# Optimization experiments

Hardware: AMD Instinct MI355X
Metric: run time of the kernel (lower is better)

The kernel has to match this reference:

```python
import jax, jax.numpy as jnp
import numpy as np

B, T, L, D, U = 2048, 500, 128, 64, 128  # batch, time steps, latent_dim, output_dim, n_units


def setup_inputs() -> dict:
    key = jax.random.key(0)
    ks = jax.random.split(key, 10)
    def init(k, shape, fan_in):
        return jax.random.uniform(k, shape, jnp.float32, -1.0, 1.0) / np.sqrt(fan_in)
    return {
        "first_point": jax.random.normal(ks[0], (1, B, L), jnp.float32),
        "time_steps_to_predict": jnp.arange(T, dtype=jnp.float32),
        # GRUCell params (torch layout: weight [3*hidden, in], gates ordered r,z,n)
        "w_ih": init(ks[1], (3 * L, D + 1), L),
        "w_hh": init(ks[2], (3 * L, L), L),
        "b_ih": init(ks[3], (3 * L,), L),
        "b_hh": init(ks[4], (3 * L,), L),
        # output_net: Linear(L,U) -> tanh -> Linear(U,D)
        "w1": init(ks[5], (U, L), L),
        "b1": jnp.zeros((U,), jnp.float32),
        "w2": init(ks[6], (D, U), U),
        "b2": jnp.zeros((D,), jnp.float32),
    }


def _gru_cell(x, h, w_ih, w_hh, b_ih, b_hh):
    gi = x @ w_ih.T + b_ih  # [B, 3L]
    gh = h @ w_hh.T + b_hh  # [B, 3L]
    i_r, i_z, i_n = jnp.split(gi, 3, axis=-1)
    h_r, h_z, h_n = jnp.split(gh, 3, axis=-1)
    r = jax.nn.sigmoid(i_r + h_r)
    z = jax.nn.sigmoid(i_z + h_z)
    n = jnp.tanh(i_n + r * h_n)
    return (1.0 - z) * n + z * h


def reference(first_point, time_steps_to_predict, w_ih, w_hh, b_ih, b_hh, w1, b1, w2, b2):
    def mlp(h):
        return jnp.tanh(h @ w1.T + b1) @ w2.T + b2  # [B, D]

    ts = time_steps_to_predict
    delta_ts = jnp.concatenate([jnp.zeros((1,), ts.dtype), ts[1:] - ts[:-1]])  # [T]

    h0 = first_point[0]          # [B, L]
    p0 = mlp(h0)                 # [B, D]
    batch = h0.shape[0]

    def step(carry, dt):
        h, p = carry
        dt_col = jnp.broadcast_to(dt.reshape(1, 1), (batch, 1))
        x = jnp.concatenate([p, dt_col], axis=-1)  # [B, D+1]
        h = _gru_cell(x, h, w_ih, w_hh, b_ih, b_hh)
        p = mlp(h)
        return (h, p), (h, p)

    _, (hs, ps) = jax.lax.scan(step, (h0, p0), delta_ts[1:])  # [T-1, B, *]
    sol_z = jnp.concatenate([h0[None], hs], axis=0)   # [T, B, L]
    pred_x = jnp.concatenate([p0[None], ps], axis=0)  # [T, B, D]
    sol_z = jnp.transpose(sol_z, (1, 0, 2))[None]     # [1, B, T, L]
    pred_x = jnp.transpose(pred_x, (1, 0, 2))[None]   # [1, B, T, D]
    return sol_z, pred_x
```

## Files before the change

kernel.cpp:

```cpp
#include <hip/hip_runtime.h>

#define BB 2048
#define TT 500
#define LL 128
#define DD 64
#define UU 128

using f16x8 = __attribute__((ext_vector_type(8))) _Float16;
using f32x4 = __attribute__((ext_vector_type(4))) float;

__device__ __forceinline__ float bf2f(unsigned short u){
  union { unsigned u; float f; } v; v.u = ((unsigned)u) << 16; return v.f;
}
__device__ __forceinline__ unsigned short f2bf(float f){
  union { float f; unsigned u; } v; v.f = f;
  unsigned r = v.u + 0x7FFFu + ((v.u >> 16) & 1u);
  return (unsigned short)(r >> 16);
}
__device__ __forceinline__ float cvt(unsigned short v){ return bf2f(v); }
__device__ __forceinline__ float cvt(float v){ return v; }

__device__ __forceinline__ float exp2_(float x){
  float r; asm("v_exp_f32 %0, %1" : "=v"(r) : "v"(x)); return r;
}

__device__ __forceinline__ void bar_lds(){
  asm volatile("s_waitcnt lgkmcnt(0)\n\ts_barrier" ::: "memory");
}

#define C1 (-1.44269504088896340736f)
#define C2 ( 2.88539008177792681472f)

#define SH 136
#define SA 136

struct Frags {
  f16x8 Wc[3][4];
  f16x8 Wh[3][4];
  f16x8 W1f[4];
  f16x8 W2f[4];
  float br, bz, bin, bhn, wdr, wdz, wdn, b1c, b2c;
};

template <typename T>
__device__ __forceinline__ void preload(
    const void* wih_, const void* whh_, const void* bih_, const void* bhh_,
    const void* w1_, const void* b1_, const void* w2_, const void* b2_,
    int c, int lq, Frags& F)
{
  const T* wih = (const T*)wih_; const T* whh = (const T*)whh_;
  const T* bih = (const T*)bih_; const T* bhh = (const T*)bhh_;
  const T* w1  = (const T*)w1_;  const T* b1  = (const T*)b1_;
  const T* w2  = (const T*)w2_;  const T* b2  = (const T*)b2_;
  const float gs[3] = {C1, C1, C2};
  #pragma unroll
  for (int g = 0; g < 3; ++g){
    const int row = g*128 + c;
    #pragma unroll
    for (int kt = 0; kt < 4; ++kt)
      #pragma unroll
      for (int j = 0; j < 8; ++j)
        F.Wh[g][kt][j] = (_Float16)(gs[g]*cvt(whh[row*128 + kt*32 + lq*8 + j]));
  }
  #pragma unroll
  for (int kt = 0; kt < 4; ++kt)
    #pragma unroll
    for (int j = 0; j < 8; ++j)
      F.W1f[kt][j] = (_Float16)(C2*cvt(w1[c*128 + kt*32 + lq*8 + j]));
  const int c2 = c & 63;
  #pragma unroll
  for (int kt = 0; kt < 4; ++kt)
    #pragma unroll
    for (int j = 0; j < 8; ++j)
      F.W2f[kt][j] = (_Float16)cvt(w2[c2*128 + kt*32 + lq*8 + j]);

  for (int kt = 0; kt < 4; ++kt){
    float acc[3][8];
    #pragma unroll
    for (int g = 0; g < 3; ++g)
      #pragma unroll
      for (int j = 0; j < 8; ++j) acc[g][j] = 0.f;
    for (int d = 0; d < 64; ++d){
      float w2r[8];
      #pragma unroll
      for (int j = 0; j < 8; ++j)
        w2r[j] = cvt(w2[d*128 + kt*32 + lq*8 + j]);
      #pragma unroll
      for (int g = 0; g < 3; ++g){
        const float wpv = cvt(wih[(g*128 + c)*65 + d]);
        #pragma unroll
        for (int j = 0; j < 8; ++j) acc[g][j] += wpv * w2r[j];
      }
    }
    #pragma unroll
    for (int g = 0; g < 3; ++g)
      #pragma unroll
      for (int j = 0; j < 8; ++j)
        F.Wc[g][kt][j] = (_Float16)(gs[g]*acc[g][j]);
  }
  float bc[3] = {0.f, 0.f, 0.f};
  for (int d = 0; d < 64; ++d){
    const float b2v = cvt(b2[d]);
    #pragma unroll
    for (int g = 0; g < 3; ++g)
      bc[g] += cvt(wih[(g*128 + c)*65 + d]) * b2v;
  }
  F.br  = C1*(cvt(bih[c])     + cvt(bhh[c])     + bc[0]);
  F.bz  = C1*(cvt(bih[128+c]) + cvt(bhh[128+c]) + bc[1]);
  F.bin = C2*(cvt(bih[256+c]) + bc[2]);
  F.bhn = C2*cvt(bhh[256+c]);
  F.wdr = C1*cvt(wih[c*65 + 64]);
  F.wdz = C1*cvt(wih[(128+c)*65 + 64]);
  F.wdn = C2*cvt(wih[(256+c)*65 + 64]);
  F.b1c = C2*cvt(b1[c]);
  F.b2c = cvt(b2[c2]);
}

__global__ __launch_bounds__(512, 2) void rnn_decoder(
    const void* __restrict__ fp0,
    const void* __restrict__ ts,
    const void* __restrict__ wih,
    const void* __restrict__ whh,
    const void* __restrict__ bih,
    const void* __restrict__ bhh,
    const void* __restrict__ w1,
    const void* __restrict__ b1,
    const void* __restrict__ w2,
    const void* __restrict__ b2,
    void* __restrict__ out)
{
  __shared__ __align__(16) _Float16 sh[16*SH];
  __shared__ __align__(16) _Float16 sa[16*SA];
  __shared__ float dts[TT];

  const int tid  = threadIdx.x;
  const int wv   = tid >> 6;
  const int lane = tid & 63;
  const int lm   = lane & 15;
  const int lq   = lane >> 4;
  const int b0   = blockIdx.x << 4;
  const int c    = (wv << 4) + lm;

  const bool isbf = (((const unsigned*)ts)[1] != 0x3F800000u);

  Frags F;
  if (isbf) preload<unsigned short>(wih, whh, bih, bhh, w1, b1, w2, b2, c, lq, F);
  else      preload<float>         (wih, whh, bih, bhh, w1, b1, w2, b2, c, lq, F);

  if (isbf){
    const unsigned short* t16 = (const unsigned short*)ts;
    for (int t = tid; t < TT; t += 512)
      dts[t] = t ? (bf2f(t16[t]) - bf2f(t16[t-1])) : 0.f;
  } else {
    const float* t32 = (const float*)ts;
    for (int t = tid; t < TT; t += 512)
      dts[t] = t ? (t32[t] - t32[t-1]) : 0.f;
  }

  unsigned short* outh16 = (unsigned short*)out;
  unsigned short* outp16 = outh16 + (size_t)BB*TT*LL;
  float* outh32 = (float*)out;
  float* outp32 = outh32 + (size_t)BB*TT*LL;

  unsigned offh[4], offp[4];
  #pragma unroll
  for (int i = 0; i < 4; ++i){
    offh[i] = (unsigned)((b0 + lq*4 + i)*TT*LL + c) + (unsigned)LL;
    offp[i] = (unsigned)((b0 + lq*4 + i)*TT*DD + (c & 63));
  }

  {
    const int row = tid >> 5;
    const int k4  = (tid & 31) << 2;
    if (isbf){
      const unsigned short* src = (const unsigned short*)fp0 + (b0 + row)*LL + k4;
      ushort4 v = *(const ushort4*)src;
      #pragma unroll
      for (int j = 0; j < 4; ++j)
        sh[row*SH + k4 + j] = (_Float16)bf2f(((const unsigned short*)&v)[j]);
      *(ushort4*)(outh16 + (size_t)(b0 + row)*TT*LL + k4) = v;
    } else {
      const float* src = (const float*)fp0 + (b0 + row)*LL + k4;
      float4 v = *(const float4*)src;
      sh[row*SH + k4 + 0] = (_Float16)v.x;
      sh[row*SH + k4 + 1] = (_Float16)v.y;
      sh[row*SH + k4 + 2] = (_Float16)v.z;
      sh[row*SH + k4 + 3] = (_Float16)v.w;
      *(float4*)(outh32 + (size_t)(b0 + row)*TT*LL + k4) = v;
    }
  }
  bar_lds();

  float hprev[4];
  #pragma unroll
  for (int i = 0; i < 4; ++i)
    hprev[i] = (float)sh[(lq*4 + i)*SH + c];

  f16x8 ahc[4], aac[4];
  #pragma unroll
  for (int kt = 0; kt < 4; ++kt)
    ahc[kt] = *(const f16x8*)&sh[lm*SH + kt*32 + lq*8];

  f32x4 aR = {0,0,0,0}, aZ = {0,0,0,0}, aH = {0,0,0,0};
  {
    f32x4 acc = {0,0,0,0};
    #pragma unroll
    for (int kt = 0; kt < 4; ++kt)
      acc = __builtin_amdgcn_mfma_f32_16x16x32_f16(ahc[kt], F.W1f[kt], acc, 0,0,0);
    #pragma unroll
    for (int kt = 0; kt < 4; ++kt){
      aR = __builtin_amdgcn_mfma_f32_16x16x32_f16(ahc[kt], F.Wh[0][kt], aR, 0,0,0);
      aZ = __builtin_amdgcn_mfma_f32_16x16x32_f16(ahc[kt], F.Wh[1][kt], aZ, 0,0,0);
      aH = __builtin_amdgcn_mfma_f32_16x16x32_f16(ahc[kt], F.Wh[2][kt], aH, 0,0,0);
    }
    #pragma unroll
    for (int i = 0; i < 4; ++i)
      sa[(lq*4 + i)*SA + c] =
        (_Float16)(1.f - 2.f*__builtin_amdgcn_rcpf(1.f + exp2_(acc[i] + F.b1c)));
  }
  bar_lds();
  #pragma unroll
  for (int kt = 0; kt < 4; ++kt)
    aac[kt] = *(const f16x8*)&sa[lm*SA + kt*32 + lq*8];

  for (int t = 1; t < TT; ++t){
    const float dt = dts[t];
    f32x4 aN = {0,0,0,0};
    #pragma unroll
    for (int kt = 0; kt < 4; ++kt){
      aR = __builtin_amdgcn_mfma_f32_16x16x32_f16(aac[kt], F.Wc[0][kt], aR, 0,0,0);
      aZ = __builtin_amdgcn_mfma_f32_16x16x32_f16(aac[kt], F.Wc[1][kt], aZ, 0,0,0);
      aN = __builtin_amdgcn_mfma_f32_16x16x32_f16(aac[kt], F.Wc[2][kt], aN, 0,0,0);
    }
    f32x4 aP = {0,0,0,0};
    if (wv < 4){
      #pragma unroll
      for (int kt = 0; kt < 4; ++kt)
        aP = __builtin_amdgcn_mfma_f32_16x16x32_f16(aac[kt], F.W2f[kt], aP, 0,0,0);
    }
    const float rb = F.br + dt*F.wdr;
    const float zb = F.bz + dt*F.wdz;
    const float nb = F.bin + dt*F.wdn;
    float hnew[4];
    #pragma unroll
    for (int i = 0; i < 4; ++i){
      const float r = __builtin_amdgcn_rcpf(1.f + exp2_(aR[i] + rb));
      const float z = __builtin_amdgcn_rcpf(1.f + exp2_(aZ[i] + zb));
      const float y = aN[i] + nb + r*(aH[i] + F.bhn);
      const float n = 1.f - 2.f*__builtin_amdgcn_rcpf(1.f + exp2_(y));
      hnew[i] = n + z*(hprev[i] - n);
      hprev[i] = hnew[i];
    }
    #pragma unroll
    for (int i = 0; i < 4; ++i)
      sh[(lq*4 + i)*SH + c] = (_Float16)hnew[i];
    bar_lds();
    #pragma unroll
    for (int kt = 0; kt < 4; ++kt)
      ahc[kt] = *(const f16x8*)&sh[lm*SH + kt*32 + lq*8];
    f32x4 acc = {0,0,0,0};
    #pragma unroll
    for (int kt = 0; kt < 4; ++kt)
      acc = __builtin_amdgcn_mfma_f32_16x16x32_f16(ahc[kt], F.W1f[kt], acc, 0,0,0);
    if (!isbf){
      #pragma unroll
      for (int i = 0; i < 4; ++i)
        outh32[offh[i]] = hnew[i];
      if (wv < 4){
        #pragma unroll
        for (int i = 0; i < 4; ++i)
          outp32[offp[i]] = aP[i] + F.b2c;
      }
    } else {
      #pragma unroll
      for (int i = 0; i < 4; ++i)
        outh16[offh[i]] = f2bf(hnew[i]);
      if (wv < 4){
        #pragma unroll
        for (int i = 0; i < 4; ++i)
          outp16[offp[i]] = f2bf(aP[i] + F.b2c);
      }
    }
    #pragma unroll
    for (int i = 0; i < 4; ++i){ offh[i] += LL; offp[i] += DD; }
    aR = (f32x4){0,0,0,0}; aZ = (f32x4){0,0,0,0}; aH = (f32x4){0,0,0,0};
    #pragma unroll
    for (int kt = 0; kt < 4; ++kt){
      aR = __builtin_amdgcn_mfma_f32_16x16x32_f16(ahc[kt], F.Wh[0][kt], aR, 0,0,0);
      aZ = __builtin_amdgcn_mfma_f32_16x16x32_f16(ahc[kt], F.Wh[1][kt], aZ, 0,0,0);
      aH = __builtin_amdgcn_mfma_f32_16x16x32_f16(ahc[kt], F.Wh[2][kt], aH, 0,0,0);
    }
    #pragma unroll
    for (int i = 0; i < 4; ++i)
      sa[(lq*4 + i)*SA + c] =
        (_Float16)(1.f - 2.f*__builtin_amdgcn_rcpf(1.f + exp2_(acc[i] + F.b1c)));
    bar_lds();
    #pragma unroll
    for (int kt = 0; kt < 4; ++kt)
      aac[kt] = *(const f16x8*)&sa[lm*SA + kt*32 + lq*8];
  }

  if (wv < 4){
    f32x4 aP = {0,0,0,0};
    #pragma unroll
    for (int kt = 0; kt < 4; ++kt)
      aP = __builtin_amdgcn_mfma_f32_16x16x32_f16(aac[kt], F.W2f[kt], aP, 0,0,0);
    if (!isbf){
      #pragma unroll
      for (int i = 0; i < 4; ++i)
        outp32[offp[i]] = aP[i] + F.b2c;
    } else {
      #pragma unroll
      for (int i = 0; i < 4; ++i)
        outp16[offp[i]] = f2bf(aP[i] + F.b2c);
    }
  }
}

extern "C" void kernel_launch(void* const* d_in, const int* in_sizes, int n_in,
                              void* d_out, int out_size, void* d_ws, size_t ws_size,
                              hipStream_t stream) {
  (void)in_sizes; (void)n_in; (void)out_size; (void)d_ws; (void)ws_size;
  rnn_decoder<<<dim3(BB/16), dim3(512), 0, stream>>>(
      d_in[0],
      d_in[1],
      d_in[2],
      d_in[3],
      d_in[4],
      d_in[5],
      d_in[6],
      d_in[7],
      d_in[8],
      d_in[9],
      d_out);
}
```

Measured before the change: 1.297 ms.

## Halve block to 4 waves, each wave computing two 16-column hidden tiles

Each block now runs 256 threads instead of 512, and each wave owns two column tiles of the hidden state (c0 and c0+64). All four waves now compute the output projection, so the wave<4 predicate is gone. The aim is to cut barrier participants and idle waves per step and to improve per-wave MFMA issue density. In exchange each wave holds twice the weight fragments in registers, which raises register pressure and allows only one block per CU via launch bounds, so there is less latency hiding.

```diff
diff --git a/kernel.cpp b/kernel.cpp
--- a/kernel.cpp
+++ b/kernel.cpp
@@ -4,7 +4,6 @@
 #define TT 500
 #define LL 128
 #define DD 64
-#define UU 128
 
 using f16x8 = __attribute__((ext_vector_type(8))) _Float16;
 using f32x4 = __attribute__((ext_vector_type(4))) float;
@@ -35,18 +34,18 @@
 #define SA 136
 
 struct Frags {
-  f16x8 Wc[3][4];
-  f16x8 Wh[3][4];
-  f16x8 W1f[4];
+  f16x8 Wc[3][2][4];
+  f16x8 Wh[3][2][4];
+  f16x8 W1f[2][4];
   f16x8 W2f[4];
-  float br, bz, bin, bhn, wdr, wdz, wdn, b1c, b2c;
+  float br[2], bz[2], bin[2], bhn[2], wdr[2], wdz[2], wdn[2], b1c[2], b2c;
 };
 
 template <typename T>
 __device__ __forceinline__ void preload(
     const void* wih_, const void* whh_, const void* bih_, const void* bhh_,
     const void* w1_, const void* b1_, const void* w2_, const void* b2_,
-    int c, int lq, Frags& F)
+    int c0, int lq, Frags& F)
 {
   const T* wih = (const T*)wih_; const T* whh = (const T*)whh_;
   const T* bih = (const T*)bih_; const T* bhh = (const T*)bhh_;
@@ -54,69 +53,72 @@
   const T* w2  = (const T*)w2_;  const T* b2  = (const T*)b2_;
   const float gs[3] = {C1, C1, C2};
   #pragma unroll
-  for (int g = 0; g < 3; ++g){
-    const int row = g*128 + c;
+  for (int ta = 0; ta < 2; ++ta){
+    const int c = c0 + 64*ta;
+    #pragma unroll
+    for (int g = 0; g < 3; ++g){
+      const int row = g*128 + c;
+      #pragma unroll
+      for (int kt = 0; kt < 4; ++kt)
+        #pragma unroll
+        for (int j = 0; j < 8; ++j)
+          F.Wh[g][ta][kt][j] = (_Float16)(gs[g]*cvt(whh[row*128 + kt*32 + lq*8 + j]));
+    }
     #pragma unroll
     for (int kt = 0; kt < 4; ++kt)
       #pragma unroll
       for (int j = 0; j < 8; ++j)
-        F.Wh[g][kt][j] = (_Float16)(gs[g]*cvt(whh[row*128 + kt*32 + lq*8 + j]));
+        F.W1f[ta][kt][j] = (_Float16)(C2*cvt(w1[c*128 + kt*32 + lq*8 + j]));
+
+    for (int kt = 0; kt < 4; ++kt){
+      float acc[3][8];
+      #pragma unroll
+      for (int g = 0; g < 3; ++g)
+        #pragma unroll
+        for (int j = 0; j < 8; ++j) acc[g][j] = 0.f;
+      for (int d = 0; d < 64; ++d){
+        float w2r[8];
+        #pragma unroll
+        for (int j = 0; j < 8; ++j)
+          w2r[j] = cvt(w2[d*128 + kt*32 + lq*8 + j]);
+        #pragma unroll
+        for (int g = 0; g < 3; ++g){
+          const float wpv = cvt(wih[(g*128 + c)*65 + d]);
+          #pragma unroll
+          for (int j = 0; j < 8; ++j) acc[g][j] += wpv * w2r[j];
+        }
+      }
+      #pragma unroll
+      for (int g = 0; g < 3; ++g)
+        #pragma unroll
+        for (int j = 0; j < 8; ++j)
+          F.Wc[g][ta][kt][j] = (_Float16)(gs[g]*acc[g][j]);
+    }
+    float bc[3] = {0.f, 0.f, 0.f};
+    for (int d = 0; d < 64; ++d){
+      const float b2v = cvt(b2[d]);
+      #pragma unroll
+      for (int g = 0; g < 3; ++g)
+        bc[g] += cvt(wih[(g*128 + c)*65 + d]) * b2v;
+    }
+    F.br[ta]  = C1*(cvt(bih[c])     + cvt(bhh[c])     + bc[0]);
+    F.bz[ta]  = C1*(cvt(bih[128+c]) + cvt(bhh[128+c]) + bc[1]);
+    F.bin[ta] = C2*(cvt(bih[256+c]) + bc[2]);
+    F.bhn[ta] = C2*cvt(bhh[256+c]);
+    F.wdr[ta] = C1*cvt(wih[c*65 + 64]);
+    F.wdz[ta] = C1*cvt(wih[(128+c)*65 + 64]);
+    F.wdn[ta] = C2*cvt(wih[(256+c)*65 + 64]);
+    F.b1c[ta] = C2*cvt(b1[c]);
   }
   #pragma unroll
   for (int kt = 0; kt < 4; ++kt)
     #pragma unroll
     for (int j = 0; j < 8; ++j)
-      F.W1f[kt][j] = (_Float16)(C2*cvt(w1[c*128 + kt*32 + lq*8 + j]));
-  const int c2 = c & 63;
-  #pragma unroll
-  for (int kt = 0; kt < 4; ++kt)
-    #pragma unroll
-    for (int j = 0; j < 8; ++j)
-      F.W2f[kt][j] = (_Float16)cvt(w2[c2*128 + kt*32 + lq*8 + j]);
-
-  for (int kt = 0; kt < 4; ++kt){
-    float acc[3][8];
-    #pragma unroll
-    for (int g = 0; g < 3; ++g)
-      #pragma unroll
-      for (int j = 0; j < 8; ++j) acc[g][j] = 0.f;
-    for (int d = 0; d < 64; ++d){
-      float w2r[8];
-      #pragma unroll
-      for (int j = 0; j < 8; ++j)
-        w2r[j] = cvt(w2[d*128 + kt*32 + lq*8 + j]);
-      #pragma unroll
-      for (int g = 0; g < 3; ++g){
-        const float wpv = cvt(wih[(g*128 + c)*65 + d]);
-        #pragma unroll
-        for (int j = 0; j < 8; ++j) acc[g][j] += wpv * w2r[j];
-      }
-    }
-    #pragma unroll
-    for (int g = 0; g < 3; ++g)
-      #pragma unroll
-      for (int j = 0; j < 8; ++j)
-        F.Wc[g][kt][j] = (_Float16)(gs[g]*acc[g][j]);
-  }
-  float bc[3] = {0.f, 0.f, 0.f};
-  for (int d = 0; d < 64; ++d){
-    const float b2v = cvt(b2[d]);
-    #pragma unroll
-    for (int g = 0; g < 3; ++g)
-      bc[g] += cvt(wih[(g*128 + c)*65 + d]) * b2v;
-  }
-  F.br  = C1*(cvt(bih[c])     + cvt(bhh[c])     + bc[0]);
-  F.bz  = C1*(cvt(bih[128+c]) + cvt(bhh[128+c]) + bc[1]);
-  F.bin = C2*(cvt(bih[256+c]) + bc[2]);
-  F.bhn = C2*cvt(bhh[256+c]);
-  F.wdr = C1*cvt(wih[c*65 + 64]);
-  F.wdz = C1*cvt(wih[(128+c)*65 + 64]);
-  F.wdn = C2*cvt(wih[(256+c)*65 + 64]);
-  F.b1c = C2*cvt(b1[c]);
-  F.b2c = cvt(b2[c2]);
-}
-
-__global__ __launch_bounds__(512, 2) void rnn_decoder(
+      F.W2f[kt][j] = (_Float16)cvt(w2[c0*128 + kt*32 + lq*8 + j]);
+  F.b2c = cvt(b2[c0]);
+}
+
+__global__ __launch_bounds__(256, 1) void rnn_decoder(
     const void* __restrict__ fp0,
     const void* __restrict__ ts,
     const void* __restrict__ wih,
@@ -139,21 +141,21 @@
   const int lm   = lane & 15;
   const int lq   = lane >> 4;
   const int b0   = blockIdx.x << 4;
-  const int c    = (wv << 4) + lm;
+  const int c0   = (wv << 4) + lm;
 
   const bool isbf = (((const unsigned*)ts)[1] != 0x3F800000u);
 
   Frags F;
-  if (isbf) preload<unsigned short>(wih, whh, bih, bhh, w1, b1, w2, b2, c, lq, F);
-  else      preload<float>         (wih, whh, bih, bhh, w1, b1, w2, b2, c, lq, F);
+  if (isbf) preload<unsigned short>(wih, whh, bih, bhh, w1, b1, w2, b2, c0, lq, F);
+  else      preload<float>         (wih, whh, bih, bhh, w1, b1, w2, b2, c0, lq, F);
 
   if (isbf){
     const unsigned short* t16 = (const unsigned short*)ts;
-    for (int t = tid; t < TT; t += 512)
+    for (int t = tid; t < TT; t += 256)
       dts[t] = t ? (bf2f(t16[t]) - bf2f(t16[t-1])) : 0.f;
   } else {
     const float* t32 = (const float*)ts;
-    for (int t = tid; t < TT; t += 512)
+    for (int t = tid; t < TT; t += 256)
       dts[t] = t ? (t32[t] - t32[t-1]) : 0.f;
   }
 
@@ -165,58 +167,74 @@
   unsigned offh[4], offp[4];
   #pragma unroll
   for (int i = 0; i < 4; ++i){
-    offh[i] = (unsigned)((b0 + lq*4 + i)*TT*LL + c) + (unsigned)LL;
-    offp[i] = (unsigned)((b0 + lq*4 + i)*TT*DD + (c & 63));
+    offh[i] = (unsigned)((b0 + lq*4 + i)*TT*LL + c0) + (unsigned)LL;
+    offp[i] = (unsigned)((b0 + lq*4 + i)*TT*DD + c0);
   }
 
   {
-    const int row = tid >> 5;
-    const int k4  = (tid & 31) << 2;
+    const int row = tid >> 4;
+    const int k8  = (tid & 15) << 3;
+    const int gb  = b0 + row;
     if (isbf){
-      const unsigned short* src = (const unsigned short*)fp0 + (b0 + row)*LL + k4;
-      ushort4 v = *(const ushort4*)src;
-      #pragma unroll
-      for (int j = 0; j < 4; ++j)
-        sh[row*SH + k4 + j] = (_Float16)bf2f(((const unsigned short*)&v)[j]);
-      *(ushort4*)(outh16 + (size_t)(b0 + row)*TT*LL + k4) = v;
+      const unsigned short* src = (const unsigned short*)fp0 + gb*LL + k8;
+      uint4 v = *(const uint4*)src;
+      f16x8 hv;
+      #pragma unroll
+      for (int j = 0; j < 8; ++j)
+        hv[j] = (_Float16)bf2f(((const unsigned short*)&v)[j]);
+      *(f16x8*)&sh[row*SH + k8] = hv;
+      *(uint4*)(outh16 + (size_t)gb*TT*LL + k8) = v;
     } else {
-      const float* src = (const float*)fp0 + (b0 + row)*LL + k4;
-      float4 v = *(const float4*)src;
-      sh[row*SH + k4 + 0] = (_Float16)v.x;
-      sh[row*SH + k4 + 1] = (_Float16)v.y;
-      sh[row*SH + k4 + 2] = (_Float16)v.z;
-      sh[row*SH + k4 + 3] = (_Float16)v.w;
-      *(float4*)(outh32 + (size_t)(b0 + row)*TT*LL + k4) = v;
+      const float* src = (const float*)fp0 + gb*LL + k8;
+      float4 v0 = *(const float4*)(src);
+      float4 v1 = *(const float4*)(src + 4);
+      f16x8 hv;
+      hv[0] = (_Float16)v0.x; hv[1] = (_Float16)v0.y;
+      hv[2] = (_Float16)v0.z; hv[3] = (_Float16)v0.w;
+      hv[4] = (_Float16)v1.x; hv[5] = (_Float16)v1.y;
+      hv[6] = (_Float16)v1.z; hv[7] = (_Float16)v1.w;
+      *(f16x8*)&sh[row*SH + k8] = hv;
+      *(float4*)(outh32 + (size_t)gb*TT*LL + k8) = v0;
+      *(float4*)(outh32 + (size_t)gb*TT*LL + k8 + 4) = v1;
     }
   }
   bar_lds();
 
-  float hprev[4];
-  #pragma unroll
-  for (int i = 0; i < 4; ++i)
-    hprev[i] = (float)sh[(lq*4 + i)*SH + c];
+  float hprev[2][4];
+  #pragma unroll
+  for (int ta = 0; ta < 2; ++ta)
+    #pragma unroll
+    for (int i = 0; i < 4; ++i)
+      hprev[ta][i] = (float)sh[(lq*4 + i)*SH + c0 + 64*ta];
 
   f16x8 ahc[4], aac[4];
   #pragma unroll
   for (int kt = 0; kt < 4; ++kt)
     ahc[kt] = *(const f16x8*)&sh[lm*SH + kt*32 + lq*8];
 
-  f32x4 aR = {0,0,0,0}, aZ = {0,0,0,0}, aH = {0,0,0,0};
+  f32x4 aRh[2], aZh[2], aHh[2];
+
   {
-    f32x4 acc = {0,0,0,0};
-    #pragma unroll
-    for (int kt = 0; kt < 4; ++kt)
-      acc = __builtin_amdgcn_mfma_f32_16x16x32_f16(ahc[kt], F.W1f[kt], acc, 0,0,0);
-    #pragma unroll
-    for (int kt = 0; kt < 4; ++kt){
-      aR = __builtin_amdgcn_mfma_f32_16x16x32_f16(ahc[kt], F.Wh[0][kt], aR, 0,0,0);
-      aZ = __builtin_amdgcn_mfma_f32_16x16x32_f16(ahc[kt], F.Wh[1][kt], aZ, 0,0,0);
-      aH = __builtin_amdgcn_mfma_f32_16x16x32_f16(ahc[kt], F.Wh[2][kt], aH, 0,0,0);
-    }
-    #pragma unroll
-    for (int i = 0; i < 4; ++i)
-      sa[(lq*4 + i)*SA + c] =
-        (_Float16)(1.f - 2.f*__builtin_amdgcn_rcpf(1.f + exp2_(acc[i] + F.b1c)));
+    f32x4 acc[2] = {{0,0,0,0},{0,0,0,0}};
+    #pragma unroll
+    for (int ta = 0; ta < 2; ++ta)
+      #pragma unroll
+      for (int kt = 0; kt < 4; ++kt)
+        acc[ta] = __builtin_amdgcn_mfma_f32_16x16x32_f16(ahc[kt], F.W1f[ta][kt], acc[ta], 0,0,0);
+    #pragma unroll
+    for (int ta = 0; ta < 2; ++ta){
+      aRh[ta] = (f32x4){0,0,0,0}; aZh[ta] = (f32x4){0,0,0,0}; aHh[ta] = (f32x4){0,0,0,0};
+      #pragma unroll
+      for (int kt = 0; kt < 4; ++kt){
+        aRh[ta] = __builtin_amdgcn_mfma_f32_16x16x32_f16(ahc[kt], F.Wh[0][ta][kt], aRh[ta], 0,0,0);
+        aZh[ta] = __builtin_amdgcn_mfma_f32_16x16x32_f16(ahc[kt], F.Wh[1][ta][kt], aZh[ta], 0,0,0);
+        aHh[ta] = __builtin_amdgcn_mfma_f32_16x16x32_f16(ahc[kt], F.Wh[2][ta][kt], aHh[ta], 0,0,0);
+      }
+      #pragma unroll
+      for (int i = 0; i < 4; ++i)
+        sa[(lq*4 + i)*SA + c0 + 64*ta] =
+          (_Float16)(1.f - 2.f*__builtin_amdgcn_rcpf(1.f + exp2_(acc[ta][i] + F.b1c[ta])));
+    }
   }
   bar_lds();
   #pragma unroll
@@ -225,82 +243,93 @@
 
   for (int t = 1; t < TT; ++t){
     const float dt = dts[t];
-    f32x4 aN = {0,0,0,0};
-    #pragma unroll
-    for (int kt = 0; kt < 4; ++kt){
-      aR = __builtin_amdgcn_mfma_f32_16x16x32_f16(aac[kt], F.Wc[0][kt], aR, 0,0,0);
-      aZ = __builtin_amdgcn_mfma_f32_16x16x32_f16(aac[kt], F.Wc[1][kt], aZ, 0,0,0);
-      aN = __builtin_amdgcn_mfma_f32_16x16x32_f16(aac[kt], F.Wc[2][kt], aN, 0,0,0);
-    }
+    float rb[2], zb[2], nb[2];
+    #pragma unroll
+    for (int ta = 0; ta < 2; ++ta){
+      rb[ta] = F.br[ta]  + dt*F.wdr[ta];
+      zb[ta] = F.bz[ta]  + dt*F.wdz[ta];
+      nb[ta] = F.bin[ta] + dt*F.wdn[ta];
+    }
+    f32x4 aRc[2] = {{0,0,0,0},{0,0,0,0}};
+    f32x4 aZc[2] = {{0,0,0,0},{0,0,0,0}};
+    f32x4 aNc[2] = {{0,0,0,0},{0,0,0,0}};
+    #pragma unroll
+    for (int ta = 0; ta < 2; ++ta)
+      #pragma unroll
+      for (int kt = 0; kt < 4; ++kt){
+        aRc[ta] = __builtin_amdgcn_mfma_f32_16x16x32_f16(aac[kt], F.Wc[0][ta][kt], aRc[ta], 0,0,0);
+        aZc[ta] = __builtin_amdgcn_mfma_f32_16x16x32_f16(aac[kt], F.Wc[1][ta][kt], aZc[ta], 0,0,0);
+        aNc[ta] = __builtin_amdgcn_mfma_f32_16x16x32_f16(aac[kt], F.Wc[2][ta][kt], aNc[ta], 0,0,0);
+      }
     f32x4 aP = {0,0,0,0};
-    if (wv < 4){
+    #pragma unroll
+    for (int kt = 0; kt < 4; ++kt)
+      aP = __builtin_amdgcn_mfma_f32_16x16x32_f16(aac[kt], F.W2f[kt], aP, 0,0,0);
+    float hnew[2][4];
+    #pragma unroll
+    for (int ta = 0; ta < 2; ++ta)
+      #pragma unroll
+      for (int i = 0; i < 4; ++i){
+        const float r = __builtin_amdgcn_rcpf(1.f + exp2_(aRh[ta][i] + aRc[ta][i] + rb[ta]));
+        const float z = __builtin_amdgcn_rcpf(1.f + exp2_(aZh[ta][i] + aZc[ta][i] + zb[ta]));
+        const float y = aNc[ta][i] + nb[ta] + r*(aHh[ta][i] + F.bhn[ta]);
+        const float n = 1.f - 2.f*__builtin_amdgcn_rcpf(1.f + exp2_(y));
+        hnew[ta][i] = n + z*(hprev[ta][i] - n);
+        hprev[ta][i] = hnew[ta][i];
+      }
+    #pragma unroll
+    for (int ta = 0; ta < 2; ++ta)
+      #pragma unroll
+      for (int i = 0; i < 4; ++i)
+        sh[(lq*4 + i)*SH + c0 + 64*ta] = (_Float16)hnew[ta][i];
+    bar_lds();
+    #pragma unroll
+    for (int kt = 0; kt < 4; ++kt)
+      ahc[kt] = *(const f16x8*)&sh[lm*SH + kt*32 + lq*8];
+    f32x4 acc[2] = {{0,0,0,0},{0,0,0,0}};
+    #pragma unroll
+    for (int ta = 0; ta < 2; ++ta)
       #pragma unroll
       for (int kt = 0; kt < 4; ++kt)
-        aP = __builtin_amdgcn_mfma_f32_16x16x32_f16(aac[kt], F.W2f[kt], aP, 0,0,0);
-    }
-    const float rb = F.br + dt*F.wdr;
-    const float zb = F.bz + dt*F.wdz;
-    const float nb = F.bin + dt*F.wdn;
-    float hnew[4];
-    #pragma unroll
-    for (int i = 0; i < 4; ++i){
-      const float r = __builtin_amdgcn_rcpf(1.f + exp2_(aR[i] + rb));
-      const float z = __builtin_amdgcn_rcpf(1.f + exp2_(aZ[i] + zb));
-      const float y = aN[i] + nb + r*(aH[i] + F.bhn);
-      const float n = 1.f - 2.f*__builtin_amdgcn_rcpf(1.f + exp2_(y));
-      hnew[i] = n + z*(hprev[i] - n);
-      hprev[i] = hnew[i];
-    }
-    #pragma unroll
-    for (int i = 0; i < 4; ++i)
-      sh[(lq*4 + i)*SH + c] = (_Float16)hnew[i];
+        acc[ta] = __builtin_amdgcn_mfma_f32_16x16x32_f16(ahc[kt], F.W1f[ta][kt], acc[ta], 0,0,0);
+    if (!isbf){
+      #pragma unroll
+      for (int i = 0; i < 4; ++i){
+        outh32[offh[i]]      = hnew[0][i];
+        outh32[offh[i] + 64] = hnew[1][i];
+        outp32[offp[i]]      = aP[i] + F.b2c;
+      }
+    } else {
+      #pragma unroll
+      for (int i = 0; i < 4; ++i){
+        outh16[offh[i]]      = f2bf(hnew[0][i]);
+        outh16[offh[i] + 64] = f2bf(hnew[1][i]);
+        outp16[offp[i]]      = f2bf(aP[i] + F.b2c);
+      }
+    }
+    #pragma unroll
+    for (int i = 0; i < 4; ++i){ offh[i] += LL; offp[i] += DD; }
+    #pragma unroll
+    for (int ta = 0; ta < 2; ++ta){
+      aRh[ta] = (f32x4){0,0,0,0}; aZh[ta] = (f32x4){0,0,0,0}; aHh[ta] = (f32x4){0,0,0,0};
+      #pragma unroll
+      for (int kt = 0; kt < 4; ++kt){
+        aRh[ta] = __builtin_amdgcn_mfma_f32_16x16x32_f16(ahc[kt], F.Wh[0][ta][kt], aRh[ta], 0,0,0);
+        aZh[ta] = __builtin_amdgcn_mfma_f32_16x16x32_f16(ahc[kt], F.Wh[1][ta][kt], aZh[ta], 0,0,0);
+        aHh[ta] = __builtin_amdgcn_mfma_f32_16x16x32_f16(ahc[kt], F.Wh[2][ta][kt], aHh[ta], 0,0,0);
+      }
+      #pragma unroll
+      for (int i = 0; i < 4; ++i)
+        sa[(lq*4 + i)*SA + c0 + 64*ta] =
+          (_Float16)(1.f - 2.f*__builtin_amdgcn_rcpf(1.f + exp2_(acc[ta][i] + F.b1c[ta])));
+    }
     bar_lds();
     #pragma unroll
     for (int kt = 0; kt < 4; ++kt)
-      ahc[kt] = *(const f16x8*)&sh[lm*SH + kt*32 + lq*8];
-    f32x4 acc = {0,0,0,0};
-    #pragma unroll
-    for (int kt = 0; kt < 4; ++kt)
-      acc = __builtin_amdgcn_mfma_f32_16x16x32_f16(ahc[kt], F.W1f[kt], acc, 0,0,0);
-    if (!isbf){
-      #pragma unroll
-      for (int i = 0; i < 4; ++i)
-        outh32[offh[i]] = hnew[i];
-      if (wv < 4){
-        #pragma unroll
-        for (int i = 0; i < 4; ++i)
-          outp32[offp[i]] = aP[i] + F.b2c;
-      }
-    } else {
-      #pragma unroll
-      for (int i = 0; i < 4; ++i)
-        outh16[offh[i]] = f2bf(hnew[i]);
-      if (wv < 4){
-        #pragma unroll
-        for (int i = 0; i < 4; ++i)
-          outp16[offp[i]] = f2bf(aP[i] + F.b2c);
-      }
-    }
-    #pragma unroll
-    for (int i = 0; i < 4; ++i){ offh[i] += LL; offp[i] += DD; }
-    aR = (f32x4){0,0,0,0}; aZ = (f32x4){0,0,0,0}; aH = (f32x4){0,0,0,0};
-    #pragma unroll
-    for (int kt = 0; kt < 4; ++kt){
-      aR = __builtin_amdgcn_mfma_f32_16x16x32_f16(ahc[kt], F.Wh[0][kt], aR, 0,0,0);
-      aZ = __builtin_amdgcn_mfma_f32_16x16x32_f16(ahc[kt], F.Wh[1][kt], aZ, 0,0,0);
-      aH = __builtin_amdgcn_mfma_f32_16x16x32_f16(ahc[kt], F.Wh[2][kt], aH, 0,0,0);
-    }
-    #pragma unroll
-    for (int i = 0; i < 4; ++i)
-      sa[(lq*4 + i)*SA + c] =
-        (_Float16)(1.f - 2.f*__builtin_amdgcn_rcpf(1.f + exp2_(acc[i] + F.b1c)));
-    bar_lds();
-    #pragma unroll
-    for (int kt = 0; kt < 4; ++kt)
       aac[kt] = *(const f16x8*)&sa[lm*SA + kt*32 + lq*8];
   }
 
-  if (wv < 4){
+  {
     f32x4 aP = {0,0,0,0};
     #pragma unroll
     for (int kt = 0; kt < 4; ++kt)
@@ -321,7 +350,7 @@
                               void* d_out, int out_size, void* d_ws, size_t ws_size,
                               hipStream_t stream) {
   (void)in_sizes; (void)n_in; (void)out_size; (void)d_ws; (void)ws_size;
-  rnn_decoder<<<dim3(BB/16), dim3(512), 0, stream>>>(
+  rnn_decoder<<<dim3(BB/16), dim3(256), 0, stream>>>(
       d_in[0],
       d_in[1],
       d_in[2],
```

Measured after the change: 1.531 ms. 18.0% more time.

## Replace folded W_ih·W2 weights with explicit prediction staging through LDS

Applied to the files above, without the earlier changes.

Removes the precomputed composite matrix Wc = W_ih[:, :64]·W2, whose preload costs a 64-step inner loop per lane. Instead, the four waves that own prediction outputs compute p = W2·a each step, write it to a new LDS buffer, and all waves then apply the original W_ih prediction block with K=64 (2 MFMA k-tiles instead of 4). This lowers per-step MFMA count and register pressure, but adds a third barrier per time step to the serial recurrence and puts the W2 matmul on the critical path.

```diff
diff --git a/kernel.cpp b/kernel.cpp
--- a/kernel.cpp
+++ b/kernel.cpp
@@ -4,7 +4,6 @@
 #define TT 500
 #define LL 128
 #define DD 64
-#define UU 128
 
 using f16x8 = __attribute__((ext_vector_type(8))) _Float16;
 using f32x4 = __attribute__((ext_vector_type(4))) float;
@@ -33,10 +32,11 @@
 
 #define SH 136
 #define SA 136
+#define SP 72
 
 struct Frags {
-  f16x8 Wc[3][4];
   f16x8 Wh[3][4];
+  f16x8 Wp[3][2];
   f16x8 W1f[4];
   f16x8 W2f[4];
   float br, bz, bin, bhn, wdr, wdz, wdn, b1c, b2c;
@@ -61,6 +61,11 @@
       #pragma unroll
       for (int j = 0; j < 8; ++j)
         F.Wh[g][kt][j] = (_Float16)(gs[g]*cvt(whh[row*128 + kt*32 + lq*8 + j]));
+    #pragma unroll
+    for (int kt = 0; kt < 2; ++kt)
+      #pragma unroll
+      for (int j = 0; j < 8; ++j)
+        F.Wp[g][kt][j] = (_Float16)(gs[g]*cvt(wih[row*65 + kt*32 + lq*8 + j]));
   }
   #pragma unroll
   for (int kt = 0; kt < 4; ++kt)
@@ -74,40 +79,9 @@
     for (int j = 0; j < 8; ++j)
       F.W2f[kt][j] = (_Float16)cvt(w2[c2*128 + kt*32 + lq*8 + j]);
 
-  for (int kt = 0; kt < 4; ++kt){
-    float acc[3][8];
-    #pragma unroll
-    for (int g = 0; g < 3; ++g)
-      #pragma unroll
-      for (int j = 0; j < 8; ++j) acc[g][j] = 0.f;
-    for (int d = 0; d < 64; ++d){
-      float w2r[8];
-      #pragma unroll
-      for (int j = 0; j < 8; ++j)
-        w2r[j] = cvt(w2[d*128 + kt*32 + lq*8 + j]);
-      #pragma unroll
-      for (int g = 0; g < 3; ++g){
-        const float wpv = cvt(wih[(g*128 + c)*65 + d]);
-        #pragma unroll
-        for (int j = 0; j < 8; ++j) acc[g][j] += wpv * w2r[j];
-      }
-    }
-    #pragma unroll
-    for (int g = 0; g < 3; ++g)
-      #pragma unroll
-      for (int j = 0; j < 8; ++j)
-        F.Wc[g][kt][j] = (_Float16)(gs[g]*acc[g][j]);
-  }
-  float bc[3] = {0.f, 0.f, 0.f};
-  for (int d = 0; d < 64; ++d){
-    const float b2v = cvt(b2[d]);
-    #pragma unroll
-    for (int g = 0; g < 3; ++g)
-      bc[g] += cvt(wih[(g*128 + c)*65 + d]) * b2v;
-  }
-  F.br  = C1*(cvt(bih[c])     + cvt(bhh[c])     + bc[0]);
-  F.bz  = C1*(cvt(bih[128+c]) + cvt(bhh[128+c]) + bc[1]);
-  F.bin = C2*(cvt(bih[256+c]) + bc[2]);
+  F.br  = C1*(cvt(bih[c])     + cvt(bhh[c]));
+  F.bz  = C1*(cvt(bih[128+c]) + cvt(bhh[128+c]));
+  F.bin = C2*cvt(bih[256+c]);
   F.bhn = C2*cvt(bhh[256+c]);
   F.wdr = C1*cvt(wih[c*65 + 64]);
   F.wdz = C1*cvt(wih[(128+c)*65 + 64]);
@@ -131,6 +105,7 @@
 {
   __shared__ __align__(16) _Float16 sh[16*SH];
   __shared__ __align__(16) _Float16 sa[16*SA];
+  __shared__ __align__(16) _Float16 sp[16*SP];
   __shared__ float dts[TT];
 
   const int tid  = threadIdx.x;
@@ -196,12 +171,13 @@
   for (int i = 0; i < 4; ++i)
     hprev[i] = (float)sh[(lq*4 + i)*SH + c];
 
-  f16x8 ahc[4], aac[4];
+  f16x8 ahc[4];
   #pragma unroll
   for (int kt = 0; kt < 4; ++kt)
     ahc[kt] = *(const f16x8*)&sh[lm*SH + kt*32 + lq*8];
 
   f32x4 aR = {0,0,0,0}, aZ = {0,0,0,0}, aH = {0,0,0,0};
+
   {
     f32x4 acc = {0,0,0,0};
     #pragma unroll
@@ -219,24 +195,39 @@
         (_Float16)(1.f - 2.f*__builtin_amdgcn_rcpf(1.f + exp2_(acc[i] + F.b1c)));
   }
   bar_lds();
-  #pragma unroll
-  for (int kt = 0; kt < 4; ++kt)
-    aac[kt] = *(const f16x8*)&sa[lm*SA + kt*32 + lq*8];
+
+  if (wv < 4){
+    f16x8 aac[4];
+    #pragma unroll
+    for (int kt = 0; kt < 4; ++kt)
+      aac[kt] = *(const f16x8*)&sa[lm*SA + kt*32 + lq*8];
+    f32x4 aP = {0,0,0,0};
+    #pragma unroll
+    for (int kt = 0; kt < 4; ++kt)
+      aP = __builtin_amdgcn_mfma_f32_16x16x32_f16(aac[kt], F.W2f[kt], aP, 0,0,0);
+    #pragma unroll
+    for (int i = 0; i < 4; ++i){
+      const float pv = aP[i] + F.b2c;
+      sp[(lq*4 + i)*SP + c] = (_Float16)pv;
+      if (!isbf) outp32[offp[i]] = pv;
+      else       outp16[offp[i]] = f2bf(pv);
+    }
+  }
+  #pragma unroll
+  for (int i = 0; i < 4; ++i) offp[i] += DD;
+  bar_lds();
 
   for (int t = 1; t < TT; ++t){
     const float dt = dts[t];
+    f16x8 pf[2];
+    pf[0] = *(const f16x8*)&sp[lm*SP + lq*8];
+    pf[1] = *(const f16x8*)&sp[lm*SP + 32 + lq*8];
     f32x4 aN = {0,0,0,0};
     #pragma unroll
-    for (int kt = 0; kt < 4; ++kt){
-      aR = __builtin_amdgcn_mfma_f32_16x16x32_f16(aac[kt], F.Wc[0][kt], aR, 0,0,0);
-      aZ = __builtin_amdgcn_mfma_f32_16x16x32_f16(aac[kt], F.Wc[1][kt], aZ, 0,0,0);
-      aN = __builtin_amdgcn_mfma_f32_16x16x32_f16(aac[kt], F.Wc[2][kt], aN, 0,0,0);
-    }
-    f32x4 aP = {0,0,0,0};
-    if (wv < 4){
-      #pragma unroll
-      for (int kt = 0; kt < 4; ++kt)
-        aP = __builtin_amdgcn_mfma_f32_16x16x32_f16(aac[kt], F.W2f[kt], aP, 0,0,0);
+    for (int kt = 0; kt < 2; ++kt){
+      aR = __builtin_amdgcn_mfma_f32_16x16x32_f16(pf[kt], F.Wp[0][kt], aR, 0,0,0);
+      aZ = __builtin_amdgcn_mfma_f32_16x16x32_f16(pf[kt], F.Wp[1][kt], aZ, 0,0,0);
+      aN = __builtin_amdgcn_mfma_f32_16x16x32_f16(pf[kt], F.Wp[2][kt], aN, 0,0,0);
     }
     const float rb = F.br + dt*F.wdr;
     const float zb = F.bz + dt*F.wdz;
@@ -266,23 +257,13 @@
       #pragma unroll
       for (int i = 0; i < 4; ++i)
         outh32[offh[i]] = hnew[i];
-      if (wv < 4){
-        #pragma unroll
-        for (int i = 0; i < 4; ++i)
-          outp32[offp[i]] = aP[i] + F.b2c;
-      }
     } else {
       #pragma unroll
       for (int i = 0; i < 4; ++i)
         outh16[offh[i]] = f2bf(hnew[i]);
-      if (wv < 4){
-        #pragma unroll
-        for (int i = 0; i < 4; ++i)
-          outp16[offp[i]] = f2bf(aP[i] + F.b2c);
-      }
-    }
-    #pragma unroll
-    for (int i = 0; i < 4; ++i){ offh[i] += LL; offp[i] += DD; }
+    }
+    #pragma unroll
+    for (int i = 0; i < 4; ++i) offh[i] += LL;
     aR = (f32x4){0,0,0,0}; aZ = (f32x4){0,0,0,0}; aH = (f32x4){0,0,0,0};
     #pragma unroll
     for (int kt = 0; kt < 4; ++kt){
@@ -295,25 +276,26 @@
       sa[(lq*4 + i)*SA + c] =
         (_Float16)(1.f - 2.f*__builtin_amdgcn_rcpf(1.f + exp2_(acc[i] + F.b1c)));
     bar_lds();
-    #pragma unroll
-    for (int kt = 0; kt < 4; ++kt)
-      aac[kt] = *(const f16x8*)&sa[lm*SA + kt*32 + lq*8];
-  }
-
-  if (wv < 4){
-    f32x4 aP = {0,0,0,0};
-    #pragma unroll
-    for (int kt = 0; kt < 4; ++kt)
-      aP = __builtin_amdgcn_mfma_f32_16x16x32_f16(aac[kt], F.W2f[kt], aP, 0,0,0);
-    if (!isbf){
-      #pragma unroll
-      for (int i = 0; i < 4; ++i)
-        outp32[offp[i]] = aP[i] + F.b2c;
-    } else {
-      #pragma unroll
-      for (int i = 0; i < 4; ++i)
-        outp16[offp[i]] = f2bf(aP[i] + F.b2c);
-    }
+    if (wv < 4){
+      f16x8 aac[4];
+      #pragma unroll
+      for (int kt = 0; kt < 4; ++kt)
+        aac[kt] = *(const f16x8*)&sa[lm*SA + kt*32 + lq*8];
+      f32x4 aP = {0,0,0,0};
+      #pragma unroll
+      for (int kt = 0; kt < 4; ++kt)
+        aP = __builtin_amdgcn_mfma_f32_16x16x32_f16(aac[kt], F.W2f[kt], aP, 0,0,0);
+      #pragma unroll
+      for (int i = 0; i < 4; ++i){
+        const float pv = aP[i] + F.b2c;
+        sp[(lq*4 + i)*SP + c] = (_Float16)pv;
+        if (!isbf) outp32[offp[i]] = pv;
+        else       outp16[offp[i]] = f2bf(pv);
+      }
+    }
+    #pragma unroll
+    for (int i = 0; i < 4; ++i) offp[i] += DD;
+    bar_lds();
   }
 }
 
```

Result: faster. 1.267 ms (-2.4%).
